# Performance work log

Hardware: AMD Instinct MI355X
Metric: run time of the kernel (lower is better)

## Reference

```python
import jax, jax.numpy as jnp
import numpy as np

B, T = 8, 512
V, H = 2048, 4
N_EMBD = 768


def setup_inputs() -> dict:
    key = jax.random.key(0)
    k1, k2, k3, k4 = jax.random.split(key, 4)
    x = jax.random.randint(k1, (B, T, 1), 0, V, dtype=jnp.int64)
    cooc = jax.random.normal(k2, (V, V, H), dtype=jnp.float32)
    proj_w = jax.random.normal(k3, (N_EMBD, V * H * H), dtype=jnp.float32) * 0.01
    proj_b = jax.random.normal(k4, (N_EMBD,), dtype=jnp.float32)
    return {"x": x, "cooc": cooc, "proj_w": proj_w, "proj_b": proj_b}


def reference(x, cooc, proj_w, proj_b):
    # x: [B,T,1] int token ids; cooc: [V,V,H]
    tok = x[..., 0]  # [B,T]
    Vv, _, Hh = cooc.shape
    Bb, Tt = tok.shape
    # att scores: wei[b,i,j,h] = cooc[tok[b,i], tok[b,j], h]  (keys index rows, queries cols)
    wei = cooc[tok[:, :, None], tok[:, None, :], :]  # [B,T,T,H]
    att = jax.nn.softmax(wei, axis=2)  # softmax over last token axis (dim=-1 of [T,T])
    att = att + jnp.eye(Tt, dtype=att.dtype)[None, :, :, None]  # self loops
    # value embedding table is flatten(cooc, 1, 2): [V, V*H]; same for every head
    v = cooc.reshape(Vv, Vv * Hh)[tok]  # [B,T,V*H]
    # per-head: att[:,:,:,h] @ v -> [B,T,V*H]; concat over heads on last dim
    out = jnp.einsum('bijh,bjd->bihd', att, v)  # [B,T,H,V*H]
    out = out.reshape(Bb, Tt, Hh * Vv * Hh)  # [B,T,H*V*H]
    # projection (dropout p=0.0 / eval mode -> identity)
    y = out @ proj_w.T + proj_b  # [B,T,n_embd]
    return y
```

## Files before the change

kernel.cpp:

```cpp
#include <hip/hip_runtime.h>
#include <stdint.h>

#define B_    8
#define T_    512
#define V_    2048
#define H_    4
#define NE_   768
#define D_    8192
#define PWROW 32768
#define M1    3072
#define K3    2048
#define MTT_E 6291456UL

typedef __attribute__((ext_vector_type(8))) short bf16x8;
typedef __attribute__((ext_vector_type(4))) float f32x4;

__device__ __forceinline__ unsigned short f2bf(float f) {
  union { float f; unsigned int u; } c; c.f = f;
  unsigned int u = c.u;
  return (unsigned short)((u + 0x7FFFu + ((u >> 16) & 1u)) >> 16);
}
__device__ __forceinline__ float bf2f(unsigned short s) {
  union { unsigned int u; float f; } c; c.u = ((unsigned int)s) << 16;
  return c.f;
}

__global__ __launch_bounds__(256) void cvtAB_k(
    const float* __restrict__ cooc, const float* __restrict__ pw,
    unsigned short* __restrict__ dst, int bq4, int n4) {
  int i = blockIdx.x * 256 + threadIdx.x;
  const int stride = gridDim.x * 256;
  for (; i < n4; i += stride) {
    const float4 v = (i < bq4) ? ((const float4*)cooc)[i]
                               : ((const float4*)pw)[i - bq4];
    ushort4 o;
    o.x = f2bf(v.x); o.y = f2bf(v.y); o.z = f2bf(v.z); o.w = f2bf(v.w);
    ((ushort4*)dst)[i] = o;
  }
}

__global__ __launch_bounds__(512, 2) void gemm1p_k(
    const unsigned short* __restrict__ Aq,
    const unsigned short* __restrict__ Bq,
    unsigned short* __restrict__ P,
    int kk_per) {
  __shared__ unsigned short lds[2][2][256 * 64];
  const int r0 = blockIdx.x * 256;
  const int t0 = blockIdx.y * 256;
  const int z  = blockIdx.z;
  const int kbeg = z * kk_per;
  const int NT = kk_per / 64;
  const int tid  = threadIdx.x;
  const int lane = tid & 63, w = tid >> 6;
  const int wm = w >> 2, wn = w & 3;
  const int fr = lane & 15, fq = lane >> 4;
  unsigned short* __restrict__ Pz = P + (size_t)z * MTT_E;

  f32x4 acc[8][4];
  #pragma unroll
  for (int m = 0; m < 8; ++m)
    #pragma unroll
    for (int n = 0; n < 4; ++n) acc[m][n] = (f32x4){0.f, 0.f, 0.f, 0.f};

  auto STAGE = [&](int d, int k0) {
    #pragma unroll
    for (int i = 0; i < 4; ++i) {
      const int q   = (w * 4 + i) * 64 + lane;
      const int row = q >> 3;
      const int c16 = (q & 7) ^ (row & 7);
      __builtin_amdgcn_global_load_lds(
          (const __attribute__((address_space(1))) void*)
              (Aq + (size_t)(r0 + row) * D_ + k0 + c16 * 8),
          (__attribute__((address_space(3))) void*)(&lds[d][0][(w * 4 + i) * 512]),
          16, 0, 0);
    }
    #pragma unroll
    for (int i = 0; i < 4; ++i) {
      const int q   = (w * 4 + i) * 64 + lane;
      const int row = q >> 3;
      const int c16 = (q & 7) ^ (row & 7);
      __builtin_amdgcn_global_load_lds(
          (const __attribute__((address_space(1))) void*)
              (Bq + (size_t)(t0 + row) * D_ + k0 + c16 * 8),
          (__attribute__((address_space(3))) void*)(&lds[d][1][(w * 4 + i) * 512]),
          16, 0, 0);
    }
  };
  #define OFFS(r, c) ((r) * 64 + (((c) ^ ((r) & 7)) * 8))

  STAGE(0, kbeg);

  for (int kt = 0; kt < NT; ++kt) {
    if (kt + 1 < NT) {
      STAGE((kt + 1) & 1, kbeg + (kt + 1) * 64);
      asm volatile("s_waitcnt vmcnt(8)" ::: "memory");
    } else {
      asm volatile("s_waitcnt vmcnt(0)" ::: "memory");
    }
    __builtin_amdgcn_s_barrier();
    __builtin_amdgcn_sched_barrier(0);

    const unsigned short* Ab = &lds[kt & 1][0][0];
    const unsigned short* Bb = &lds[kt & 1][1][0];

    bf16x8 afA[4][2], afB[4][2], bf0[2][2], bf1[2][2];
    #pragma unroll
    for (int m = 0; m < 4; ++m)
      #pragma unroll
      for (int kk = 0; kk < 2; ++kk)
        afA[m][kk] = *(const bf16x8*)&Ab[OFFS(wm * 128 + m * 16 + fr, kk * 4 + fq)];
    #pragma unroll
    for (int n = 0; n < 2; ++n)
      #pragma unroll
      for (int kk = 0; kk < 2; ++kk) {
        bf0[n][kk] = *(const bf16x8*)&Bb[OFFS(wn * 64 + n * 16 + fr, kk * 4 + fq)];
        bf1[n][kk] = *(const bf16x8*)&Bb[OFFS(wn * 64 + 32 + n * 16 + fr, kk * 4 + fq)];
      }

    __builtin_amdgcn_s_setprio(1);
    #pragma unroll
    for (int m = 0; m < 4; ++m)
      #pragma unroll
      for (int n = 0; n < 2; ++n)
        #pragma unroll
        for (int kk = 0; kk < 2; ++kk) {
          acc[m][n]     = __builtin_amdgcn_mfma_f32_16x16x32_bf16(afA[m][kk], bf0[n][kk], acc[m][n], 0, 0, 0);
          acc[m][n + 2] = __builtin_amdgcn_mfma_f32_16x16x32_bf16(afA[m][kk], bf1[n][kk], acc[m][n + 2], 0, 0, 0);
        }
    #pragma unroll
    for (int m = 0; m < 4; ++m)
      #pragma unroll
      for (int kk = 0; kk < 2; ++kk)
        afB[m][kk] = *(const bf16x8*)&Ab[OFFS(wm * 128 + 64 + m * 16 + fr, kk * 4 + fq)];
    #pragma unroll
    for (int m = 0; m < 4; ++m)
      #pragma unroll
      for (int n = 0; n < 2; ++n)
        #pragma unroll
        for (int kk = 0; kk < 2; ++kk) {
          acc[m + 4][n]     = __builtin_amdgcn_mfma_f32_16x16x32_bf16(afB[m][kk], bf0[n][kk], acc[m + 4][n], 0, 0, 0);
          acc[m + 4][n + 2] = __builtin_amdgcn_mfma_f32_16x16x32_bf16(afB[m][kk], bf1[n][kk], acc[m + 4][n + 2], 0, 0, 0);
        }
    __builtin_amdgcn_s_setprio(0);

    __builtin_amdgcn_s_barrier();
    __builtin_amdgcn_sched_barrier(0);
  }
  #undef OFFS

  #pragma unroll
  for (int m = 0; m < 8; ++m)
    #pragma unroll
    for (int n = 0; n < 4; ++n) {
      const int rbase = r0 + wm * 128 + m * 16 + fq * 4;
      const int t = t0 + wn * 64 + n * 16 + fr;
      ushort4 o;
      o.x = f2bf(acc[m][n][0]); o.y = f2bf(acc[m][n][1]);
      o.z = f2bf(acc[m][n][2]); o.w = f2bf(acc[m][n][3]);
      *(ushort4*)&Pz[(size_t)(rbase >> 2) * D_ + t * H_] = o;
    }
}

__global__ __launch_bounds__(256) void gemm1f_k(
    const unsigned short* __restrict__ Aq,
    const unsigned short* __restrict__ Bq,
    unsigned short* __restrict__ P, int kk) {
  __shared__ unsigned short As[128 * 32];
  __shared__ unsigned short Bs[128 * 32];
  const int r0 = blockIdx.x * 128;
  const int t0 = blockIdx.y * 128;
  const int z  = blockIdx.z;
  const int kbeg = z * kk, kend = kbeg + kk;
  const int tid  = threadIdx.x;
  const int lane = tid & 63, wave = tid >> 6;
  const int wr = wave >> 1, wc = wave & 1;
  const int fr = lane & 15, fq = lane >> 4;
  const int l4 = lane >> 2, lb = lane & 3;
  unsigned short* __restrict__ Pz = P + (size_t)z * MTT_E;

  f32x4 acc[4][4];
  #pragma unroll
  for (int m = 0; m < 4; ++m)
    #pragma unroll
    for (int n = 0; n < 4; ++n) acc[m][n] = (f32x4){0.f, 0.f, 0.f, 0.f};

  for (int k0 = kbeg; k0 < kend; k0 += 32) {
    __syncthreads();
    #pragma unroll
    for (int c = 0; c < 2; ++c) {
      const int ch  = wave * 2 + c;
      const int row = ch * 16 + l4;
      __builtin_amdgcn_global_load_lds(
          (const __attribute__((address_space(1))) void*)
              (Aq + (size_t)(r0 + row) * D_ + k0 + lb * 8),
          (__attribute__((address_space(3))) void*)(As + ch * 512), 16, 0, 0);
      __builtin_amdgcn_global_load_lds(
          (const __attribute__((address_space(1))) void*)
              (Bq + (size_t)(t0 + row) * D_ + k0 + lb * 8),
          (__attribute__((address_space(3))) void*)(Bs + ch * 512), 16, 0, 0);
    }
    __syncthreads();
    bf16x8 af[4], bf[4];
    #pragma unroll
    for (int m = 0; m < 4; ++m)
      af[m] = *(const bf16x8*)&As[(wr * 64 + m * 16 + fr) * 32 + fq * 8];
    #pragma unroll
    for (int n = 0; n < 4; ++n)
      bf[n] = *(const bf16x8*)&Bs[(wc * 64 + n * 16 + fr) * 32 + fq * 8];
    #pragma unroll
    for (int m = 0; m < 4; ++m)
      #pragma unroll
      for (int n = 0; n < 4; ++n)
        acc[m][n] = __builtin_amdgcn_mfma_f32_16x16x32_bf16(af[m], bf[n], acc[m][n], 0, 0, 0);
  }
  #pragma unroll
  for (int m = 0; m < 4; ++m)
    #pragma unroll
    for (int n = 0; n < 4; ++n) {
      const int rbase = r0 + wr * 64 + m * 16 + fq * 4;
      const int t = t0 + wc * 64 + n * 16 + fr;
      ushort4 o;
      o.x = f2bf(acc[m][n][0]); o.y = f2bf(acc[m][n][1]);
      o.z = f2bf(acc[m][n][2]); o.w = f2bf(acc[m][n][3]);
      *(ushort4*)&Pz[(size_t)(rbase >> 2) * D_ + t * H_] = o;
    }
}

__global__ __launch_bounds__(256) void reduceN_k(
    unsigned short* __restrict__ P0, int nz) {
  const size_t i = ((size_t)blockIdx.x * 256 + threadIdx.x) * 8;
  float s[8];
  {
    ushort4 a0 = *(const ushort4*)(P0 + i);
    ushort4 a1 = *(const ushort4*)(P0 + i + 4);
    s[0] = bf2f(a0.x); s[1] = bf2f(a0.y); s[2] = bf2f(a0.z); s[3] = bf2f(a0.w);
    s[4] = bf2f(a1.x); s[5] = bf2f(a1.y); s[6] = bf2f(a1.z); s[7] = bf2f(a1.w);
  }
  for (int z = 1; z < nz; ++z) {
    const unsigned short* Pz = P0 + (size_t)z * MTT_E;
    ushort4 b0 = *(const ushort4*)(Pz + i);
    ushort4 b1 = *(const ushort4*)(Pz + i + 4);
    s[0] += bf2f(b0.x); s[1] += bf2f(b0.y); s[2] += bf2f(b0.z); s[3] += bf2f(b0.w);
    s[4] += bf2f(b1.x); s[5] += bf2f(b1.y); s[6] += bf2f(b1.z); s[7] += bf2f(b1.w);
  }
  ushort4 o0, o1;
  o0.x = f2bf(s[0]); o0.y = f2bf(s[1]); o0.z = f2bf(s[2]); o0.w = f2bf(s[3]);
  o1.x = f2bf(s[4]); o1.y = f2bf(s[5]); o1.z = f2bf(s[6]); o1.w = f2bf(s[7]);
  *(ushort4*)(P0 + i) = o0;
  *(ushort4*)(P0 + i + 4) = o1;
}

__global__ __launch_bounds__(256) void gather_k(
    const unsigned short* __restrict__ mtT, const int* __restrict__ x,
    unsigned short* __restrict__ GT) {
  __shared__ int toks[B_ * T_];
  const int tid = threadIdx.x;
  #pragma unroll
  for (int c = 0; c < 16; ++c) toks[c * 256 + tid] = x[c * 256 + tid];
  __syncthreads();

  const int lane = tid & 63, wave = tid >> 6;
  const int e = blockIdx.x * 4 + wave;
  const unsigned short* mrow = mtT + (size_t)e * D_;
  #pragma unroll
  for (int b = 0; b < B_; ++b) {
    unsigned short* grow = GT + ((size_t)b * NE_ + e) * K3;
    const int* tb = toks + b * T_;
    #pragma unroll
    for (int r = 0; r < 8; ++r) {
      const int j = r * 64 + lane;
      const uint2 v = *(const uint2*)(mrow + (size_t)tb[j] * H_);
      *(uint2*)(grow + j * H_) = v;
    }
  }
}

__global__ __launch_bounds__(256) void gemm3f_k(
    const unsigned short* __restrict__ att,
    const unsigned short* __restrict__ GT,
    const float* __restrict__ bias,
    float* __restrict__ y) {
  __shared__ unsigned short As[128 * 32];
  __shared__ unsigned short Bs[64 * 32];
  const int b  = blockIdx.z;
  const int i0 = blockIdx.x * 128;
  const int e0 = blockIdx.y * 64;
  const int tid  = threadIdx.x;
  const int lane = tid & 63, wave = tid >> 6;
  const int wr = wave >> 1, wc = wave & 1;
  const int fr = lane & 15, fq = lane >> 4;

  f32x4 acc[4][2];
  #pragma unroll
  for (int m = 0; m < 4; ++m)
    #pragma unroll
    for (int n = 0; n < 2; ++n) acc[m][n] = (f32x4){0.f, 0.f, 0.f, 0.f};

  const unsigned short* aB = att + (size_t)(b * T_ + i0) * K3;
  const unsigned short* bB = GT + ((size_t)b * NE_ + e0) * K3;

  for (int k0 = 0; k0 < K3; k0 += 32) {
    __syncthreads();
    #pragma unroll
    for (int rdi = 0; rdi < 2; ++rdi) {
      const int q = rdi * 256 + tid;
      const int row = q >> 2, koff = (q & 3) * 8;
      __builtin_amdgcn_global_load_lds(
          (const __attribute__((address_space(1))) void*)
              (aB + (size_t)row * K3 + k0 + koff),
          (__attribute__((address_space(3))) void*)(As + q * 8), 16, 0, 0);
    }
    {
      const int q = tid;
      const int row = q >> 2, koff = (q & 3) * 8;
      __builtin_amdgcn_global_load_lds(
          (const __attribute__((address_space(1))) void*)
              (bB + (size_t)row * K3 + k0 + koff),
          (__attribute__((address_space(3))) void*)(Bs + q * 8), 16, 0, 0);
    }
    __syncthreads();
    bf16x8 af[4], bf[2];
    #pragma unroll
    for (int m = 0; m < 4; ++m)
      af[m] = *(const bf16x8*)&As[(wr * 64 + m * 16 + fr) * 32 + fq * 8];
    #pragma unroll
    for (int n = 0; n < 2; ++n)
      bf[n] = *(const bf16x8*)&Bs[(wc * 32 + n * 16 + fr) * 32 + fq * 8];
    #pragma unroll
    for (int m = 0; m < 4; ++m)
      #pragma unroll
      for (int n = 0; n < 2; ++n)
        acc[m][n] = __builtin_amdgcn_mfma_f32_16x16x32_bf16(af[m], bf[n], acc[m][n], 0, 0, 0);
  }

  #pragma unroll
  for (int m = 0; m < 4; ++m)
    #pragma unroll
    for (int n = 0; n < 2; ++n) {
      const int i = i0 + wr * 64 + m * 16 + fq * 4;
      const int e = e0 + wc * 32 + n * 16 + fr;
      const float be = bias[e];
      #pragma unroll
      for (int g = 0; g < 4; ++g)
        y[(size_t)(b * T_ + i + g) * NE_ + e] = acc[m][n][g] + be;
    }
}

__global__ __launch_bounds__(64) void softmax_k(
    const int* __restrict__ x, const float* __restrict__ cooc,
    unsigned short* __restrict__ att) {
  const int bi = blockIdx.x;
  const int b = bi >> 9, i = bi & (T_ - 1);
  const int lane = threadIdx.x;
  const int ti = x[b * T_ + i];
  const float* crow = cooc + (size_t)ti * D_;

  float w[8][4];
  #pragma unroll
  for (int r = 0; r < 8; ++r) {
    const int j = lane + r * 64;
    const int tj = x[b * T_ + j];
    const float4 v = *(const float4*)(crow + (size_t)tj * H_);
    w[r][0] = v.x; w[r][1] = v.y; w[r][2] = v.z; w[r][3] = v.w;
  }
  float m[4] = {-1e30f, -1e30f, -1e30f, -1e30f};
  #pragma unroll
  for (int r = 0; r < 8; ++r)
    #pragma unroll
    for (int h = 0; h < 4; ++h) m[h] = fmaxf(m[h], w[r][h]);
  #pragma unroll
  for (int off = 32; off > 0; off >>= 1)
    #pragma unroll
    for (int h = 0; h < 4; ++h) m[h] = fmaxf(m[h], __shfl_xor(m[h], off));
  float s[4] = {0.f, 0.f, 0.f, 0.f};
  #pragma unroll
  for (int r = 0; r < 8; ++r)
    #pragma unroll
    for (int h = 0; h < 4; ++h) { w[r][h] = __expf(w[r][h] - m[h]); s[h] += w[r][h]; }
  #pragma unroll
  for (int off = 32; off > 0; off >>= 1)
    #pragma unroll
    for (int h = 0; h < 4; ++h) s[h] += __shfl_xor(s[h], off);
  float inv[4];
  #pragma unroll
  for (int h = 0; h < 4; ++h) inv[h] = 1.f / s[h];

  unsigned short* arow = att + (size_t)(b * T_ + i) * (T_ * H_);
  #pragma unroll
  for (int r = 0; r < 8; ++r) {
    const int j = lane + r * 64;
    const float d = (j == i) ? 1.f : 0.f;
    ushort4 o;
    o.x = f2bf(w[r][0] * inv[0] + d);
    o.y = f2bf(w[r][1] * inv[1] + d);
    o.z = f2bf(w[r][2] * inv[2] + d);
    o.w = f2bf(w[r][3] * inv[3] + d);
    *(ushort4*)(arow + (size_t)j * H_) = o;
  }
}

__global__ __launch_bounds__(256) void gemm1_k(
    const float* __restrict__ pw, const float* __restrict__ cooc,
    unsigned short* __restrict__ mtT) {
  __shared__ unsigned short As[128 * 32];
  __shared__ unsigned short Bs[64 * 32];
  const int h  = blockIdx.z;
  const int e0 = blockIdx.x * 128;
  const int t0 = blockIdx.y * 64;
  const int tid  = threadIdx.x;
  const int lane = tid & 63, wave = tid >> 6;
  const int wr = wave >> 1, wc = wave & 1;
  const int fr = lane & 15, fq = lane >> 4;

  f32x4 acc[4][2];
  #pragma unroll
  for (int m = 0; m < 4; ++m)
    #pragma unroll
    for (int n = 0; n < 2; ++n) acc[m][n] = (f32x4){0.f, 0.f, 0.f, 0.f};

  const float* aB = pw + (size_t)e0 * PWROW + (size_t)h * D_;
  const float* bB = cooc + (size_t)t0 * D_;

  for (int k0 = 0; k0 < D_; k0 += 32) {
    __syncthreads();
    #pragma unroll
    for (int c = 0; c < 4; ++c) {
      const int fe = (c * 256 + tid) * 4;
      const int row = fe >> 5, k = fe & 31;
      const float4 v = *(const float4*)(aB + (size_t)row * PWROW + k0 + k);
      ushort4 o; o.x = f2bf(v.x); o.y = f2bf(v.y); o.z = f2bf(v.z); o.w = f2bf(v.w);
      *(ushort4*)&As[fe] = o;
    }
    #pragma unroll
    for (int c = 0; c < 2; ++c) {
      const int fe = (c * 256 + tid) * 4;
      const int row = fe >> 5, k = fe & 31;
      const float4 v = *(const float4*)(bB + (size_t)row * D_ + k0 + k);
      ushort4 o; o.x = f2bf(v.x); o.y = f2bf(v.y); o.z = f2bf(v.z); o.w = f2bf(v.w);
      *(ushort4*)&Bs[fe] = o;
    }
    __syncthreads();
    bf16x8 af[4], bf[2];
    #pragma unroll
    for (int m = 0; m < 4; ++m)
      af[m] = *(const bf16x8*)&As[(wr * 64 + m * 16 + fr) * 32 + fq * 8];
    #pragma unroll
    for (int n = 0; n < 2; ++n)
      bf[n] = *(const bf16x8*)&Bs[(wc * 32 + n * 16 + fr) * 32 + fq * 8];
    #pragma unroll
    for (int m = 0; m < 4; ++m)
      #pragma unroll
      for (int n = 0; n < 2; ++n)
        acc[m][n] = __builtin_amdgcn_mfma_f32_16x16x32_bf16(af[m], bf[n], acc[m][n], 0, 0, 0);
  }
  #pragma unroll
  for (int m = 0; m < 4; ++m)
    #pragma unroll
    for (int n = 0; n < 2; ++n) {
      const int e = e0 + wr * 64 + m * 16 + fq * 4;
      const int t = t0 + wc * 32 + n * 16 + fr;
      #pragma unroll
      for (int g = 0; g < 4; ++g)
        mtT[(size_t)(e + g) * D_ + t * H_ + h] = f2bf(acc[m][n][g]);
    }
}

__global__ __launch_bounds__(256) void gemm3_k(
    const unsigned short* __restrict__ att, const unsigned short* __restrict__ mtT,
    const int* __restrict__ x, const float* __restrict__ bias,
    float* __restrict__ y) {
  __shared__ unsigned short As[64 * 32];
  __shared__ unsigned short Bs[128 * 32];
  const int b  = blockIdx.z;
  const int i0 = blockIdx.x * 64;
  const int e0 = blockIdx.y * 128;
  const int tid  = threadIdx.x;
  const int lane = tid & 63, wave = tid >> 6;
  const int wr = wave >> 1, wc = wave & 1;
  const int fr = lane & 15, fq = lane >> 4;

  f32x4 acc[2][4];
  #pragma unroll
  for (int m = 0; m < 2; ++m)
    #pragma unroll
    for (int n = 0; n < 4; ++n) acc[m][n] = (f32x4){0.f, 0.f, 0.f, 0.f};

  const unsigned short* aB = att + (size_t)(b * T_ + i0) * (T_ * H_);

  for (int ks = 0; ks < 64; ++ks) {
    const int k0 = ks * 32;
    __syncthreads();
    {
      const int fe = tid * 8;
      const int row = fe >> 5, k = fe & 31;
      const uint4 v = *(const uint4*)(aB + (size_t)row * (T_ * H_) + k0 + k);
      *(uint4*)&As[fe] = v;
    }
    #pragma unroll
    for (int c = 0; c < 4; ++c) {
      const int q = c * 256 + tid;
      const int n = q >> 3, j8 = q & 7;
      const int tj = x[b * T_ + ks * 8 + j8];
      const uint2 v = *(const uint2*)(mtT + (size_t)(e0 + n) * D_ + tj * H_);
      *(uint2*)&Bs[n * 32 + j8 * 4] = v;
    }
    __syncthreads();
    bf16x8 af[2], bf[4];
    #pragma unroll
    for (int m = 0; m < 2; ++m)
      af[m] = *(const bf16x8*)&As[(wr * 32 + m * 16 + fr) * 32 + fq * 8];
    #pragma unroll
    for (int n = 0; n < 4; ++n)
      bf[n] = *(const bf16x8*)&Bs[(wc * 64 + n * 16 + fr) * 32 + fq * 8];
    #pragma unroll
    for (int m = 0; m < 2; ++m)
      #pragma unroll
      for (int n = 0; n < 4; ++n)
        acc[m][n] = __builtin_amdgcn_mfma_f32_16x16x32_bf16(af[m], bf[n], acc[m][n], 0, 0, 0);
  }
  #pragma unroll
  for (int m = 0; m < 2; ++m)
    #pragma unroll
    for (int n = 0; n < 4; ++n) {
      const int i = i0 + wr * 32 + m * 16 + fq * 4;
      const int e = e0 + wc * 64 + n * 16 + fr;
      const float be = bias[e];
      #pragma unroll
      for (int g = 0; g < 4; ++g)
        y[(size_t)(b * T_ + i + g) * NE_ + e] = acc[m][n][g] + be;
    }
}

extern "C" void kernel_launch(void* const* d_in, const int* in_sizes, int n_in,
                              void* d_out, int out_size, void* d_ws, size_t ws_size,
                              hipStream_t stream) {
  const int*   x    = (const int*)d_in[0];
  const float* cooc = (const float*)d_in[1];
  const float* pw   = (const float*)d_in[2];
  const float* pb   = (const float*)d_in[3];
  float* y = (float*)d_out;

  const size_t BQ_E = (size_t)V_ * D_;
  const size_t AQ_E = (size_t)M1 * D_;

  unsigned short* mtT = (unsigned short*)d_ws;
  auto need = [&](int c) { return ((size_t)c * MTT_E + BQ_E + AQ_E) * 2; };

  int nz = 0, pipe = 0;
  if      (ws_size >= need(8)) { nz = 8; pipe = 1; }
  else if (ws_size >= need(4)) { nz = 4; pipe = 1; }
  else if (ws_size >= need(2)) { nz = 2; pipe = 0; }
  else if (ws_size >= need(1)) { nz = 1; pipe = 0; }

  if (nz >= 1) {
    unsigned short* Bq  = mtT + (size_t)nz * MTT_E;
    unsigned short* Aq  = Bq + BQ_E;
    unsigned short* GT  = Bq;
    unsigned short* att = Aq;
    hipLaunchKernelGGL(cvtAB_k, dim3(2048), dim3(256), 0, stream,
                       cooc, pw, Bq, (int)(BQ_E / 4), (int)((BQ_E + AQ_E) / 4));
    if (pipe)
      hipLaunchKernelGGL(gemm1p_k, dim3(M1 / 256, V_ / 256, nz), dim3(512), 0,
                         stream, Aq, Bq, mtT, D_ / nz);
    else
      hipLaunchKernelGGL(gemm1f_k, dim3(M1 / 128, V_ / 128, nz), dim3(256), 0,
                         stream, Aq, Bq, mtT, D_ / nz);
    if (nz > 1)
      hipLaunchKernelGGL(reduceN_k, dim3((unsigned)(MTT_E / (256 * 8))), dim3(256),
                         0, stream, mtT, nz);
    hipLaunchKernelGGL(softmax_k, dim3(B_ * T_), dim3(64), 0, stream, x, cooc, att);
    hipLaunchKernelGGL(gather_k, dim3(NE_ / 4), dim3(256), 0, stream, mtT, x, GT);
    hipLaunchKernelGGL(gemm3f_k, dim3(T_ / 128, NE_ / 64, B_), dim3(256), 0, stream,
                       att, GT, pb, y);
  } else {
    unsigned short* att = mtT + MTT_E;
    hipLaunchKernelGGL(gemm1_k, dim3(NE_ / 128, V_ / 64, H_), dim3(256), 0, stream,
                       pw, cooc, mtT);
    hipLaunchKernelGGL(softmax_k, dim3(B_ * T_), dim3(64), 0, stream, x, cooc, att);
    hipLaunchKernelGGL(gemm3_k, dim3(T_ / 64, NE_ / 128, B_), dim3(256), 0, stream,
                       att, mtT, x, pb, y);
  }
}
```

Before: 242.1 us.

## Interleave half-tile prefetch with MFMA quadrants and fuse split-K reduction into gather

The main GEMM kernel now splits each LDS stage into half-tile loads and issues them between four MFMA sub-blocks, with barriers between phases. This is meant to overlap global-to-LDS traffic with compute more finely than the previous whole-tile double buffering. The separate split-K reduction kernel is removed, and the gather kernel sums the nz partial slices only at the gathered token positions. That drops a full pass over the partial buffers, but the gather now does scattered reads across nz slices and adds more barriers per iteration.

After: 410.8 us. +69.7%, slower.

```diff
diff --git a/kernel.cpp b/kernel.cpp
--- a/kernel.cpp
+++ b/kernel.cpp
@@ -11,6 +11,9 @@
 #define M1    3072
 #define K3    2048
 #define MTT_E 6291456UL
+
+#define AS1 __attribute__((address_space(1)))
+#define AS3 __attribute__((address_space(3)))
 
 typedef __attribute__((ext_vector_type(8))) short bf16x8;
 typedef __attribute__((ext_vector_type(4))) float f32x4;
@@ -39,7 +42,7 @@
   }
 }
 
-__global__ __launch_bounds__(512, 2) void gemm1p_k(
+__global__ __launch_bounds__(512, 2) void gemm1x_k(
     const unsigned short* __restrict__ Aq,
     const unsigned short* __restrict__ Bq,
     unsigned short* __restrict__ P,
@@ -62,101 +65,127 @@
     #pragma unroll
     for (int n = 0; n < 4; ++n) acc[m][n] = (f32x4){0.f, 0.f, 0.f, 0.f};
 
-  auto STAGE = [&](int d, int k0) {
-    #pragma unroll
-    for (int i = 0; i < 4; ++i) {
-      const int q   = (w * 4 + i) * 64 + lane;
+  auto SHALF = [&](int d, int op, int h, int k0) {
+    const unsigned short* G = op ? Bq : Aq;
+    const int base0 = op ? t0 : r0;
+    #pragma unroll
+    for (int i = 0; i < 2; ++i) {
+      const int q   = h * 1024 + (w * 2 + i) * 64 + lane;
       const int row = q >> 3;
       const int c16 = (q & 7) ^ (row & 7);
       __builtin_amdgcn_global_load_lds(
-          (const __attribute__((address_space(1))) void*)
-              (Aq + (size_t)(r0 + row) * D_ + k0 + c16 * 8),
-          (__attribute__((address_space(3))) void*)(&lds[d][0][(w * 4 + i) * 512]),
-          16, 0, 0);
-    }
-    #pragma unroll
-    for (int i = 0; i < 4; ++i) {
-      const int q   = (w * 4 + i) * 64 + lane;
-      const int row = q >> 3;
-      const int c16 = (q & 7) ^ (row & 7);
-      __builtin_amdgcn_global_load_lds(
-          (const __attribute__((address_space(1))) void*)
-              (Bq + (size_t)(t0 + row) * D_ + k0 + c16 * 8),
-          (__attribute__((address_space(3))) void*)(&lds[d][1][(w * 4 + i) * 512]),
+          (const AS1 void*)(G + (size_t)(base0 + row) * D_ + k0 + c16 * 8),
+          (AS3 void*)(&lds[d][op][(h * 1024 + (w * 2 + i) * 64) * 8]),
           16, 0, 0);
     }
   };
   #define OFFS(r, c) ((r) * 64 + (((c) ^ ((r) & 7)) * 8))
-
-  STAGE(0, kbeg);
-
-  for (int kt = 0; kt < NT; ++kt) {
-    if (kt + 1 < NT) {
-      STAGE((kt + 1) & 1, kbeg + (kt + 1) * 64);
-      asm volatile("s_waitcnt vmcnt(8)" ::: "memory");
-    } else {
-      asm volatile("s_waitcnt vmcnt(0)" ::: "memory");
-    }
-    __builtin_amdgcn_s_barrier();
-    __builtin_amdgcn_sched_barrier(0);
-
-    const unsigned short* Ab = &lds[kt & 1][0][0];
-    const unsigned short* Bb = &lds[kt & 1][1][0];
-
-    bf16x8 afA[4][2], afB[4][2], bf0[2][2], bf1[2][2];
+  #define FENCE_BAR() do { __builtin_amdgcn_sched_barrier(0); \
+                           __builtin_amdgcn_s_barrier(); \
+                           __builtin_amdgcn_sched_barrier(0); } while (0)
+
+  SHALF(0, 0, 0, kbeg); SHALF(0, 0, 1, kbeg);
+  SHALF(0, 1, 0, kbeg); SHALF(0, 1, 1, kbeg);
+  asm volatile("s_waitcnt vmcnt(0)" ::: "memory");
+  FENCE_BAR();
+
+  for (int t = 0; t < NT; ++t) {
+    const int cur = t & 1, nxt = cur ^ 1;
+    const bool hasnext = (t + 1 < NT);
+    const int kn = kbeg + (t + 1) * 64;
+    const unsigned short* Ab = &lds[cur][0][0];
+    const unsigned short* Bb = &lds[cur][1][0];
+    bf16x8 a[4][2], a2[4][2], b0[2][2], b1[2][2], b0b[2][2];
+
+    if (hasnext) { SHALF(nxt, 0, 0, kn); SHALF(nxt, 1, 0, kn); }
     #pragma unroll
     for (int m = 0; m < 4; ++m)
       #pragma unroll
       for (int kk = 0; kk < 2; ++kk)
-        afA[m][kk] = *(const bf16x8*)&Ab[OFFS(wm * 128 + m * 16 + fr, kk * 4 + fq)];
+        a[m][kk] = *(const bf16x8*)&Ab[OFFS(wm * 128 + m * 16 + fr, kk * 4 + fq)];
     #pragma unroll
     for (int n = 0; n < 2; ++n)
       #pragma unroll
-      for (int kk = 0; kk < 2; ++kk) {
-        bf0[n][kk] = *(const bf16x8*)&Bb[OFFS(wn * 64 + n * 16 + fr, kk * 4 + fq)];
-        bf1[n][kk] = *(const bf16x8*)&Bb[OFFS(wn * 64 + 32 + n * 16 + fr, kk * 4 + fq)];
-      }
-
+      for (int kk = 0; kk < 2; ++kk)
+        b0[n][kk] = *(const bf16x8*)&Bb[OFFS(wn * 64 + n * 16 + fr, kk * 4 + fq)];
+    FENCE_BAR();
     __builtin_amdgcn_s_setprio(1);
     #pragma unroll
     for (int m = 0; m < 4; ++m)
       #pragma unroll
       for (int n = 0; n < 2; ++n)
         #pragma unroll
-        for (int kk = 0; kk < 2; ++kk) {
-          acc[m][n]     = __builtin_amdgcn_mfma_f32_16x16x32_bf16(afA[m][kk], bf0[n][kk], acc[m][n], 0, 0, 0);
-          acc[m][n + 2] = __builtin_amdgcn_mfma_f32_16x16x32_bf16(afA[m][kk], bf1[n][kk], acc[m][n + 2], 0, 0, 0);
-        }
-    #pragma unroll
-    for (int m = 0; m < 4; ++m)
+        for (int kk = 0; kk < 2; ++kk)
+          acc[m][n] = __builtin_amdgcn_mfma_f32_16x16x32_bf16(a[m][kk], b0[n][kk], acc[m][n], 0, 0, 0);
+    __builtin_amdgcn_s_setprio(0);
+    FENCE_BAR();
+
+    if (hasnext) SHALF(nxt, 1, 1, kn);
+    #pragma unroll
+    for (int n = 0; n < 2; ++n)
       #pragma unroll
       for (int kk = 0; kk < 2; ++kk)
-        afB[m][kk] = *(const bf16x8*)&Ab[OFFS(wm * 128 + 64 + m * 16 + fr, kk * 4 + fq)];
+        b1[n][kk] = *(const bf16x8*)&Bb[OFFS(wn * 64 + 32 + n * 16 + fr, kk * 4 + fq)];
+    FENCE_BAR();
+    __builtin_amdgcn_s_setprio(1);
     #pragma unroll
     for (int m = 0; m < 4; ++m)
       #pragma unroll
       for (int n = 0; n < 2; ++n)
         #pragma unroll
-        for (int kk = 0; kk < 2; ++kk) {
-          acc[m + 4][n]     = __builtin_amdgcn_mfma_f32_16x16x32_bf16(afB[m][kk], bf0[n][kk], acc[m + 4][n], 0, 0, 0);
-          acc[m + 4][n + 2] = __builtin_amdgcn_mfma_f32_16x16x32_bf16(afB[m][kk], bf1[n][kk], acc[m + 4][n + 2], 0, 0, 0);
-        }
+        for (int kk = 0; kk < 2; ++kk)
+          acc[m][n + 2] = __builtin_amdgcn_mfma_f32_16x16x32_bf16(a[m][kk], b1[n][kk], acc[m][n + 2], 0, 0, 0);
     __builtin_amdgcn_s_setprio(0);
-
-    __builtin_amdgcn_s_barrier();
-    __builtin_amdgcn_sched_barrier(0);
+    FENCE_BAR();
+
+    if (hasnext) SHALF(nxt, 0, 1, kn);
+    #pragma unroll
+    for (int m = 0; m < 4; ++m)
+      #pragma unroll
+      for (int kk = 0; kk < 2; ++kk)
+        a2[m][kk] = *(const bf16x8*)&Ab[OFFS(wm * 128 + 64 + m * 16 + fr, kk * 4 + fq)];
+    FENCE_BAR();
+    __builtin_amdgcn_s_setprio(1);
+    #pragma unroll
+    for (int m = 0; m < 4; ++m)
+      #pragma unroll
+      for (int n = 0; n < 2; ++n)
+        #pragma unroll
+        for (int kk = 0; kk < 2; ++kk)
+          acc[m + 4][n + 2] = __builtin_amdgcn_mfma_f32_16x16x32_bf16(a2[m][kk], b1[n][kk], acc[m + 4][n + 2], 0, 0, 0);
+    __builtin_amdgcn_s_setprio(0);
+    FENCE_BAR();
+
+    #pragma unroll
+    for (int n = 0; n < 2; ++n)
+      #pragma unroll
+      for (int kk = 0; kk < 2; ++kk)
+        b0b[n][kk] = *(const bf16x8*)&Bb[OFFS(wn * 64 + n * 16 + fr, kk * 4 + fq)];
+    asm volatile("s_waitcnt vmcnt(0)" ::: "memory");
+    FENCE_BAR();
+    __builtin_amdgcn_s_setprio(1);
+    #pragma unroll
+    for (int m = 0; m < 4; ++m)
+      #pragma unroll
+      for (int n = 0; n < 2; ++n)
+        #pragma unroll
+        for (int kk = 0; kk < 2; ++kk)
+          acc[m + 4][n] = __builtin_amdgcn_mfma_f32_16x16x32_bf16(a2[m][kk], b0b[n][kk], acc[m + 4][n], 0, 0, 0);
+    __builtin_amdgcn_s_setprio(0);
+    FENCE_BAR();
   }
   #undef OFFS
-
-  #pragma unroll
-  for (int m = 0; m < 8; ++m)
-    #pragma unroll
-    for (int n = 0; n < 4; ++n) {
-      const int rbase = r0 + wm * 128 + m * 16 + fq * 4;
-      const int t = t0 + wn * 64 + n * 16 + fr;
+  #undef FENCE_BAR
+
+  #pragma unroll
+  for (int mi = 0; mi < 8; ++mi)
+    #pragma unroll
+    for (int ni = 0; ni < 4; ++ni) {
+      const int rbase = r0 + wm * 128 + (mi >> 2) * 64 + (mi & 3) * 16 + fq * 4;
+      const int t = t0 + wn * 64 + (ni >> 1) * 32 + (ni & 1) * 16 + fr;
       ushort4 o;
-      o.x = f2bf(acc[m][n][0]); o.y = f2bf(acc[m][n][1]);
-      o.z = f2bf(acc[m][n][2]); o.w = f2bf(acc[m][n][3]);
+      o.x = f2bf(acc[mi][ni][0]); o.y = f2bf(acc[mi][ni][1]);
+      o.z = f2bf(acc[mi][ni][2]); o.w = f2bf(acc[mi][ni][3]);
       *(ushort4*)&Pz[(size_t)(rbase >> 2) * D_ + t * H_] = o;
     }
 }
@@ -191,13 +220,11 @@
       const int ch  = wave * 2 + c;
       const int row = ch * 16 + l4;
       __builtin_amdgcn_global_load_lds(
-          (const __attribute__((address_space(1))) void*)
-              (Aq + (size_t)(r0 + row) * D_ + k0 + lb * 8),
-          (__attribute__((address_space(3))) void*)(As + ch * 512), 16, 0, 0);
+          (const AS1 void*)(Aq + (size_t)(r0 + row) * D_ + k0 + lb * 8),
+          (AS3 void*)(As + ch * 512), 16, 0, 0);
       __builtin_amdgcn_global_load_lds(
-          (const __attribute__((address_space(1))) void*)
-              (Bq + (size_t)(t0 + row) * D_ + k0 + lb * 8),
-          (__attribute__((address_space(3))) void*)(Bs + ch * 512), 16, 0, 0);
+          (const AS1 void*)(Bq + (size_t)(t0 + row) * D_ + k0 + lb * 8),
+          (AS3 void*)(Bs + ch * 512), 16, 0, 0);
     }
     __syncthreads();
     bf16x8 af[4], bf[4];
@@ -226,33 +253,9 @@
     }
 }
 
-__global__ __launch_bounds__(256) void reduceN_k(
-    unsigned short* __restrict__ P0, int nz) {
-  const size_t i = ((size_t)blockIdx.x * 256 + threadIdx.x) * 8;
-  float s[8];
-  {
-    ushort4 a0 = *(const ushort4*)(P0 + i);
-    ushort4 a1 = *(const ushort4*)(P0 + i + 4);
-    s[0] = bf2f(a0.x); s[1] = bf2f(a0.y); s[2] = bf2f(a0.z); s[3] = bf2f(a0.w);
-    s[4] = bf2f(a1.x); s[5] = bf2f(a1.y); s[6] = bf2f(a1.z); s[7] = bf2f(a1.w);
-  }
-  for (int z = 1; z < nz; ++z) {
-    const unsigned short* Pz = P0 + (size_t)z * MTT_E;
-    ushort4 b0 = *(const ushort4*)(Pz + i);
-    ushort4 b1 = *(const ushort4*)(Pz + i + 4);
-    s[0] += bf2f(b0.x); s[1] += bf2f(b0.y); s[2] += bf2f(b0.z); s[3] += bf2f(b0.w);
-    s[4] += bf2f(b1.x); s[5] += bf2f(b1.y); s[6] += bf2f(b1.z); s[7] += bf2f(b1.w);
-  }
-  ushort4 o0, o1;
-  o0.x = f2bf(s[0]); o0.y = f2bf(s[1]); o0.z = f2bf(s[2]); o0.w = f2bf(s[3]);
-  o1.x = f2bf(s[4]); o1.y = f2bf(s[5]); o1.z = f2bf(s[6]); o1.w = f2bf(s[7]);
-  *(ushort4*)(P0 + i) = o0;
-  *(ushort4*)(P0 + i + 4) = o1;
-}
-
-__global__ __launch_bounds__(256) void gather_k(
-    const unsigned short* __restrict__ mtT, const int* __restrict__ x,
-    unsigned short* __restrict__ GT) {
+__global__ __launch_bounds__(256) void gatherR_k(
+    const unsigned short* __restrict__ P, const int* __restrict__ x,
+    unsigned short* __restrict__ GT, int nz) {
   __shared__ int toks[B_ * T_];
   const int tid = threadIdx.x;
   #pragma unroll
@@ -260,17 +263,25 @@
   __syncthreads();
 
   const int lane = tid & 63, wave = tid >> 6;
-  const int e = blockIdx.x * 4 + wave;
-  const unsigned short* mrow = mtT + (size_t)e * D_;
-  #pragma unroll
-  for (int b = 0; b < B_; ++b) {
+  const int e = blockIdx.x;
+  const unsigned short* mrow = P + (size_t)e * D_;
+  #pragma unroll
+  for (int bb = 0; bb < 2; ++bb) {
+    const int b = wave * 2 + bb;
     unsigned short* grow = GT + ((size_t)b * NE_ + e) * K3;
     const int* tb = toks + b * T_;
     #pragma unroll
     for (int r = 0; r < 8; ++r) {
       const int j = r * 64 + lane;
-      const uint2 v = *(const uint2*)(mrow + (size_t)tb[j] * H_);
-      *(uint2*)(grow + j * H_) = v;
+      const int off = tb[j] * H_;
+      float s0 = 0.f, s1 = 0.f, s2 = 0.f, s3 = 0.f;
+      for (int zz = 0; zz < nz; ++zz) {
+        const ushort4 v = *(const ushort4*)(mrow + (size_t)zz * MTT_E + off);
+        s0 += bf2f(v.x); s1 += bf2f(v.y); s2 += bf2f(v.z); s3 += bf2f(v.w);
+      }
+      ushort4 o;
+      o.x = f2bf(s0); o.y = f2bf(s1); o.z = f2bf(s2); o.w = f2bf(s3);
+      *(ushort4*)(grow + j * H_) = o;
     }
   }
 }
@@ -306,17 +317,15 @@
       const int q = rdi * 256 + tid;
       const int row = q >> 2, koff = (q & 3) * 8;
       __builtin_amdgcn_global_load_lds(
-          (const __attribute__((address_space(1))) void*)
-              (aB + (size_t)row * K3 + k0 + koff),
-          (__attribute__((address_space(3))) void*)(As + q * 8), 16, 0, 0);
+          (const AS1 void*)(aB + (size_t)row * K3 + k0 + koff),
+          (AS3 void*)(As + q * 8), 16, 0, 0);
     }
     {
       const int q = tid;
       const int row = q >> 2, koff = (q & 3) * 8;
       __builtin_amdgcn_global_load_lds(
-          (const __attribute__((address_space(1))) void*)
-              (bB + (size_t)row * K3 + k0 + koff),
-          (__attribute__((address_space(3))) void*)(Bs + q * 8), 16, 0, 0);
+          (const AS1 void*)(bB + (size_t)row * K3 + k0 + koff),
+          (AS3 void*)(Bs + q * 8), 16, 0, 0);
     }
     __syncthreads();
     bf16x8 af[4], bf[2];
@@ -560,16 +569,13 @@
     hipLaunchKernelGGL(cvtAB_k, dim3(2048), dim3(256), 0, stream,
                        cooc, pw, Bq, (int)(BQ_E / 4), (int)((BQ_E + AQ_E) / 4));
     if (pipe)
-      hipLaunchKernelGGL(gemm1p_k, dim3(M1 / 256, V_ / 256, nz), dim3(512), 0,
+      hipLaunchKernelGGL(gemm1x_k, dim3(M1 / 256, V_ / 256, nz), dim3(512), 0,
                          stream, Aq, Bq, mtT, D_ / nz);
     else
       hipLaunchKernelGGL(gemm1f_k, dim3(M1 / 128, V_ / 128, nz), dim3(256), 0,
                          stream, Aq, Bq, mtT, D_ / nz);
-    if (nz > 1)
-      hipLaunchKernelGGL(reduceN_k, dim3((unsigned)(MTT_E / (256 * 8))), dim3(256),
-                         0, stream, mtT, nz);
     hipLaunchKernelGGL(softmax_k, dim3(B_ * T_), dim3(64), 0, stream, x, cooc, att);
-    hipLaunchKernelGGL(gather_k, dim3(NE_ / 4), dim3(256), 0, stream, mtT, x, GT);
+    hipLaunchKernelGGL(gatherR_k, dim3(NE_), dim3(256), 0, stream, mtT, x, GT, nz);
     hipLaunchKernelGGL(gemm3f_k, dim3(T_ / 128, NE_ / 64, B_), dim3(256), 0, stream,
                        att, GT, pb, y);
   } else {
```
